# Kernel tuning notes

Measured on AMD Instinct MI355X. Metric: run time of the kernel, lower is better.

Reference implementation:

```python
import jax, jax.numpy as jnp
import numpy as np


def _gcn_conv(x, edge_index, W, b):
    """PyG GCNConv: add self-loops, symmetric normalization, scatter-add aggregation."""
    N = x.shape[0]
    loops = jnp.arange(N, dtype=edge_index.dtype)
    src = jnp.concatenate([edge_index[0], loops])  # [E+N]
    dst = jnp.concatenate([edge_index[1], loops])  # [E+N]
    # degree computed on destination nodes (flow: source_to_target)
    deg = jax.ops.segment_sum(jnp.ones_like(dst, dtype=x.dtype), dst, num_segments=N)
    deg_inv_sqrt = jnp.where(deg > 0, jax.lax.rsqrt(jnp.maximum(deg, 1.0)), 0.0)
    norm = deg_inv_sqrt[src] * deg_inv_sqrt[dst]  # [E+N]
    h = x @ W  # [N, out]
    msg = h[src] * norm[:, None]  # [E+N, out]
    out = jax.ops.segment_sum(msg, dst, num_segments=N)
    return out + b


def setup_inputs() -> dict:
    key = jax.random.key(0)
    k1, k2, k3, k4 = jax.random.split(key, 4)
    N, E, D_IN, D_HID, D_OUT = 100000, 1600000, 128, 128, 64
    x = jax.random.normal(k1, (N, D_IN), dtype=jnp.float32)
    edge_index = jax.random.randint(k2, (2, E), 0, N, dtype=jnp.int64)
    batch = jnp.zeros((N,), dtype=jnp.int64)
    W1 = jax.random.normal(k3, (D_IN, D_HID), dtype=jnp.float32) / np.sqrt(D_IN)
    b1 = jnp.zeros((D_HID,), dtype=jnp.float32)
    W2 = jax.random.normal(k4, (D_HID, D_OUT), dtype=jnp.float32) / np.sqrt(D_HID)
    b2 = jnp.zeros((D_OUT,), dtype=jnp.float32)
    return {"x": x, "edge_index": edge_index, "batch": batch,
            "W1": W1, "b1": b1, "W2": W2, "b2": b2}


def reference(x, edge_index, batch, W1, b1, W2, b2):
    h = _gcn_conv(x, edge_index, W1, b1)
    h = jax.nn.relu(h)
    # dropout is identity at inference (training=False)
    out = _gcn_conv(h, edge_index, W2, b2)
    # original computes F.log_softmax but discards it; returns out
    return out
```

## Files before the change

### kernel.cpp

```cpp
#include <hip/hip_runtime.h>
#include <hip/hip_fp16.h>


#define KDIM 128
#define BSHIFT 9
#define BSIZE 512
#define ECHUNK 2048
#define CAP 10240
#define PACK_SHIFT 20
#define PACK_MASK ((1u << PACK_SHIFT) - 1)

typedef _Float16 h8 __attribute__((ext_vector_type(8)));
typedef float f4v __attribute__((ext_vector_type(4)));


__launch_bounds__(256) __global__
void bscatter_kernel(const int* __restrict__ src, const int* __restrict__ dst,
                     int* __restrict__ ecnt, unsigned int* __restrict__ packed_out,
                     int E, int NB) {
    __shared__ int lcnt[256];
    __shared__ int lexc[256];
    __shared__ int lbase[256];
    __shared__ unsigned int lpacked[ECHUNK];
    __shared__ unsigned char lbslot[ECHUNK];

    const int t = threadIdx.x;
    lcnt[t] = 0;
    __syncthreads();

    const int base = blockIdx.x * ECHUNK;
    const int cnt = min(ECHUNK, E - base);

#pragma unroll
    for (int j = 0; j < ECHUNK / 256; j++) {
        int e = base + j * 256 + t;
        if (e < E) atomicAdd(&lcnt[dst[e] >> BSHIFT], 1);
    }
    __syncthreads();

    lexc[t] = lcnt[t];
    __syncthreads();
    for (int off = 1; off < 256; off <<= 1) {
        int x = (t >= off) ? lexc[t - off] : 0;
        __syncthreads();
        if (t >= off) lexc[t] += x;
        __syncthreads();
    }
    lexc[t] = lexc[t] - lcnt[t];

    if (t < NB && lcnt[t]) lbase[t] = t * CAP + atomicAdd(&ecnt[t], lcnt[t]);
    __syncthreads();
    lcnt[t] = lexc[t];
    __syncthreads();

#pragma unroll
    for (int j = 0; j < ECHUNK / 256; j++) {
        int e = base + j * 256 + t;
        if (e < E) {
            int d = dst[e];
            int b = d >> BSHIFT;
            int pos = atomicAdd(&lcnt[b], 1);
            lpacked[pos] = (unsigned int)src[e] | ((unsigned int)(d & (BSIZE - 1)) << PACK_SHIFT);
            lbslot[pos] = (unsigned char)b;
        }
    }
    __syncthreads();

#pragma unroll
    for (int j = 0; j < ECHUNK / 256; j++) {
        int s = j * 256 + t;
        if (s < cnt) {
            int b = lbslot[s];
            int pos = lbase[b] + (s - lexc[b]);
            if (pos < (b + 1) * CAP)
                packed_out[pos] = lpacked[s];
        }
    }
}


__launch_bounds__(1024) __global__
void bfinal_kernel(const unsigned int* __restrict__ packed, const int* __restrict__ ecnt,
                   int* __restrict__ rowptr, float* __restrict__ dinv,
                   int* __restrict__ ssrc, int N, int E, int NB) {
    __shared__ int ncnt[BSIZE];
    __shared__ int sbuf[BSIZE];
    __shared__ int bsc[256];
    __shared__ int bbase_sh;

    const int t = threadIdx.x;
    const int b = blockIdx.x;

    if (t < 256) bsc[t] = (t < NB) ? min(ecnt[t], CAP) : 0;
    if (t < BSIZE) ncnt[t] = 0;
    __syncthreads();

    const int cnt = min(ecnt[b], CAP);
    const unsigned int* pb = packed + (size_t)b * CAP;
    unsigned int held[CAP / 1024];
#pragma unroll
    for (int j = 0; j < CAP / 1024; j++) {
        int e = t + j * 1024;
        if (e < cnt) {
            unsigned int p = pb[e];
            held[j] = p;
            atomicAdd(&ncnt[p >> PACK_SHIFT], 1);
        }
    }

    __syncthreads();
    for (int off = 1; off < 256; off <<= 1) {
        int x = 0;
        if (t < 256 && t >= off) x = bsc[t - off];
        __syncthreads();
        if (t < 256 && t >= off) bsc[t] += x;
        __syncthreads();
    }
    if (t == 0) bbase_sh = (b == 0) ? 0 : bsc[b - 1];

    int mycnt = 0;
    if (t < BSIZE) {
        mycnt = ncnt[t];
        sbuf[t] = mycnt;
    }
    __syncthreads();
    for (int off = 1; off < BSIZE; off <<= 1) {
        int x = 0;
        if (t < BSIZE && t >= off) x = sbuf[t - off];
        __syncthreads();
        if (t < BSIZE && t >= off) sbuf[t] += x;
        __syncthreads();
    }

    const int gb = bbase_sh;
    if (t < BSIZE) {
        int exc = (t == 0) ? 0 : sbuf[t - 1];
        int node = (b << BSHIFT) + t;
        if (node < N) {
            rowptr[node] = gb + exc;
            dinv[node] = rsqrtf((float)(mycnt + 1));
        }
        ncnt[t] = gb + exc;
    }
    if (t == 0 && b == NB - 1) rowptr[N] = gb + cnt;
    __syncthreads();

#pragma unroll
    for (int j = 0; j < CAP / 1024; j++) {
        int e = t + j * 1024;
        if (e < cnt) {
            unsigned int p = held[j];
            int d = p >> PACK_SHIFT;
            int pos = atomicAdd(&ncnt[d], 1);
            ssrc[pos] = (int)(p & PACK_MASK);
        }
    }
}


__device__ inline h8 pack8(float4 u, float4 v) {
    h8 r;
    r[0] = (_Float16)u.x; r[1] = (_Float16)u.y; r[2] = (_Float16)u.z; r[3] = (_Float16)u.w;
    r[4] = (_Float16)v.x; r[5] = (_Float16)v.y; r[6] = (_Float16)v.z; r[7] = (_Float16)v.w;
    return r;
}

template <int DOUT, bool AHALF>
__launch_bounds__(256) __global__
void gemm_mfma_kernel(const void* __restrict__ Xv, const float* __restrict__ W,
                      const float* __restrict__ dinv, _Float16* __restrict__ outh, int N) {
    constexpr int K = KDIM;
    constexpr int KS = K + 8;
    constexpr int NT = DOUT / 16;
    __shared__ _Float16 Wl[DOUT * KS];

    const int t = threadIdx.x;
    const int wave = t >> 6;
    const int lane = t & 63;
    const int l15 = lane & 15;
    const int quad = lane >> 4;

#pragma unroll
    for (int i = t; i < DOUT * (K / 4); i += 256) {
        int n = i & (DOUT - 1);
        int kg = i / DOUT;
        union { _Float16 h[4]; uint2 u; } tmp;
#pragma unroll
        for (int j = 0; j < 4; j++)
            tmp.h[j] = (_Float16)W[(size_t)(kg * 4 + j) * DOUT + n];
        *(uint2*)(&Wl[n * KS + kg * 4]) = tmp.u;
    }
    __syncthreads();

    const int rowbase = blockIdx.x * 128;
    const int row0 = rowbase + wave * 32 + l15;
    const int row1 = row0 + 16;
    const int rc0 = min(row0, N - 1);
    const int rc1 = min(row1, N - 1);

    f4v acc[2][NT];
#pragma unroll
    for (int r = 0; r < 2; r++)
#pragma unroll
        for (int ct = 0; ct < NT; ct++) acc[r][ct] = (f4v)0.0f;

#pragma unroll
    for (int kc = 0; kc < K; kc += 32) {
        const int kof = kc + quad * 8;
        h8 a0, a1;
        if (AHALF) {
            const _Float16* Xh = (const _Float16*)Xv;
            a0 = *(const h8*)(Xh + (size_t)rc0 * K + kof);
            a1 = *(const h8*)(Xh + (size_t)rc1 * K + kof);
        } else {
            const float* Xf = (const float*)Xv;
            const float* p0 = Xf + (size_t)rc0 * K + kof;
            const float* p1 = Xf + (size_t)rc1 * K + kof;
            a0 = pack8(*(const float4*)p0, *(const float4*)(p0 + 4));
            a1 = pack8(*(const float4*)p1, *(const float4*)(p1 + 4));
        }
#pragma unroll
        for (int ct = 0; ct < NT; ct++) {
            h8 b = *(const h8*)(&Wl[(size_t)(ct * 16 + l15) * KS + kof]);
            acc[0][ct] = __builtin_amdgcn_mfma_f32_16x16x32_f16(a0, b, acc[0][ct], 0, 0, 0);
            acc[1][ct] = __builtin_amdgcn_mfma_f32_16x16x32_f16(a1, b, acc[1][ct], 0, 0, 0);
        }
    }

#pragma unroll
    for (int r = 0; r < 2; r++) {
        const int rb = rowbase + wave * 32 + r * 16 + quad * 4;
#pragma unroll
        for (int g = 0; g < 4; g++) {
            int row = rb + g;
            if (row < N) {
                float di = dinv[row];
                _Float16* op = outh + (size_t)row * DOUT + l15;
#pragma unroll
                for (int ct = 0; ct < NT; ct++)
                    op[ct * 16] = (_Float16)(acc[r][ct][g] * di);
            }
        }
    }
}


__launch_bounds__(512, 8) __global__
void agg_gemm_kernel(const __half* __restrict__ hs, const int* __restrict__ rowptr,
                     const int* __restrict__ ssrc, const float* __restrict__ dinv,
                     const float* __restrict__ bias, const float* __restrict__ W2,
                     _Float16* __restrict__ hs2, int N) {
    constexpr int K = KDIM;
    constexpr int KS = K + 8;
    constexpr int DO2 = 64;
    __shared__ _Float16 W2l[DO2 * KS];
    __shared__ _Float16 o_lds[8][4 * KS];

    const int t = threadIdx.x;

#pragma unroll
    for (int i = t; i < DO2 * (K / 4); i += 512) {
        int n = i & (DO2 - 1);
        int kg = i >> 6;
        union { _Float16 h[4]; uint2 u; } tmp;
#pragma unroll
        for (int j = 0; j < 4; j++)
            tmp.h[j] = (_Float16)W2[(size_t)(kg * 4 + j) * DO2 + n];
        *(uint2*)(&W2l[n * KS + kg * 4]) = tmp.u;
    }
    __syncthreads();

    const int nl = t >> 4;
    const int node = blockIdx.x * 32 + nl;
    const int flane = t & 15;
    const int c0 = flane * 8;

    h8 oh;
    if (node < N) {
        float acc[8];
        {
            uint4 u = *(const uint4*)(hs + (size_t)node * K + c0);
            const __half2* hp = (const __half2*)&u;
#pragma unroll
            for (int q = 0; q < 4; q++) {
                float2 f = __half22float2(hp[q]);
                acc[2 * q] = f.x;
                acc[2 * q + 1] = f.y;
            }
        }

        const int e0 = rowptr[node];
        const int e1 = rowptr[node + 1];
        int e = e0;
        for (; e + 4 <= e1; e += 4) {
            int s0 = ssrc[e + 0];
            int s1 = ssrc[e + 1];
            int s2 = ssrc[e + 2];
            int s3 = ssrc[e + 3];
            uint4 u0 = *(const uint4*)(hs + (size_t)s0 * K + c0);
            uint4 u1 = *(const uint4*)(hs + (size_t)s1 * K + c0);
            uint4 u2 = *(const uint4*)(hs + (size_t)s2 * K + c0);
            uint4 u3 = *(const uint4*)(hs + (size_t)s3 * K + c0);
            const __half2* p0 = (const __half2*)&u0;
            const __half2* p1 = (const __half2*)&u1;
            const __half2* p2 = (const __half2*)&u2;
            const __half2* p3 = (const __half2*)&u3;
#pragma unroll
            for (int q = 0; q < 4; q++) {
                float2 f0 = __half22float2(p0[q]);
                float2 f1 = __half22float2(p1[q]);
                float2 f2 = __half22float2(p2[q]);
                float2 f3 = __half22float2(p3[q]);
                acc[2 * q]     += (f0.x + f1.x) + (f2.x + f3.x);
                acc[2 * q + 1] += (f0.y + f1.y) + (f2.y + f3.y);
            }
        }
        for (; e < e1; e++) {
            int s = ssrc[e];
            uint4 u = *(const uint4*)(hs + (size_t)s * K + c0);
            const __half2* hp = (const __half2*)&u;
#pragma unroll
            for (int q = 0; q < 4; q++) {
                float2 f = __half22float2(hp[q]);
                acc[2 * q] += f.x;
                acc[2 * q + 1] += f.y;
            }
        }

        const float di = dinv[node];
#pragma unroll
        for (int q = 0; q < 2; q++) {
            float4 bq = *(const float4*)(bias + c0 + 4 * q);
            oh[4 * q + 0] = (_Float16)fmaxf(di * acc[4 * q + 0] + bq.x, 0.f);
            oh[4 * q + 1] = (_Float16)fmaxf(di * acc[4 * q + 1] + bq.y, 0.f);
            oh[4 * q + 2] = (_Float16)fmaxf(di * acc[4 * q + 2] + bq.z, 0.f);
            oh[4 * q + 3] = (_Float16)fmaxf(di * acc[4 * q + 3] + bq.w, 0.f);
        }
    } else {
#pragma unroll
        for (int j = 0; j < 8; j++) oh[j] = (_Float16)0.f;
    }

    const int wv = t >> 6;
    const int a = (t >> 4) & 3;
    *(h8*)(&o_lds[wv][a * KS + c0]) = oh;
    asm volatile("s_waitcnt lgkmcnt(0)" ::: "memory");
    __builtin_amdgcn_sched_barrier(0);

    const int lane = t & 63;
    const int l15 = lane & 15;
    const int quad = lane >> 4;

    f4v acc2[4];
#pragma unroll
    for (int ct = 0; ct < 4; ct++) acc2[ct] = (f4v)0.0f;

#pragma unroll
    for (int kc = 0; kc < K; kc += 32) {
        const int kof = kc + quad * 8;
        h8 afr = *(const h8*)(&o_lds[wv][(l15 & 3) * KS + kof]);
#pragma unroll
        for (int ct = 0; ct < 4; ct++) {
            h8 b = *(const h8*)(&W2l[(size_t)(ct * 16 + l15) * KS + kof]);
            acc2[ct] = __builtin_amdgcn_mfma_f32_16x16x32_f16(afr, b, acc2[ct], 0, 0, 0);
        }
    }

    f4v av = (quad == 0) ? acc2[0] : (quad == 1) ? acc2[1]
           : (quad == 2) ? acc2[2] : acc2[3];
    const int rowbase = blockIdx.x * 32 + wv * 4;
#pragma unroll
    for (int g = 0; g < 4; g++) {
        int r = rowbase + g;
        if (r < N)
            hs2[(size_t)r * DO2 + quad * 16 + l15] = (_Float16)(av[g] * dinv[r]);
    }
}


template <int DOUT, bool RELU, bool HOUT>
__launch_bounds__(256) __global__
void agg_kernel(const __half* __restrict__ hs, const int* __restrict__ rowptr,
                const int* __restrict__ ssrc, const float* __restrict__ dinv,
                const float* __restrict__ bias, void* __restrict__ outv, int N) {
    constexpr int TPN = DOUT / 8;
    const int npb = blockDim.x / TPN;
    const int node = blockIdx.x * npb + threadIdx.x / TPN;
    if (node >= N) return;
    const int lane = threadIdx.x % TPN;
    const int c0 = lane * 8;

    float acc[8];
    {
        uint4 u = *(const uint4*)(hs + (size_t)node * DOUT + c0);
        const __half2* hp = (const __half2*)&u;
#pragma unroll
        for (int q = 0; q < 4; q++) {
            float2 f = __half22float2(hp[q]);
            acc[2 * q] = f.x;
            acc[2 * q + 1] = f.y;
        }
    }

    const int e0 = rowptr[node];
    const int e1 = rowptr[node + 1];
    int e = e0;
    for (; e + 4 <= e1; e += 4) {
        int s0 = ssrc[e + 0];
        int s1 = ssrc[e + 1];
        int s2 = ssrc[e + 2];
        int s3 = ssrc[e + 3];
        uint4 u0 = *(const uint4*)(hs + (size_t)s0 * DOUT + c0);
        uint4 u1 = *(const uint4*)(hs + (size_t)s1 * DOUT + c0);
        uint4 u2 = *(const uint4*)(hs + (size_t)s2 * DOUT + c0);
        uint4 u3 = *(const uint4*)(hs + (size_t)s3 * DOUT + c0);
        const __half2* p0 = (const __half2*)&u0;
        const __half2* p1 = (const __half2*)&u1;
        const __half2* p2 = (const __half2*)&u2;
        const __half2* p3 = (const __half2*)&u3;
#pragma unroll
        for (int q = 0; q < 4; q++) {
            float2 f0 = __half22float2(p0[q]);
            float2 f1 = __half22float2(p1[q]);
            float2 f2 = __half22float2(p2[q]);
            float2 f3 = __half22float2(p3[q]);
            acc[2 * q]     += (f0.x + f1.x) + (f2.x + f3.x);
            acc[2 * q + 1] += (f0.y + f1.y) + (f2.y + f3.y);
        }
    }
    for (; e < e1; e++) {
        int s = ssrc[e];
        uint4 u = *(const uint4*)(hs + (size_t)s * DOUT + c0);
        const __half2* hp = (const __half2*)&u;
#pragma unroll
        for (int q = 0; q < 4; q++) {
            float2 f = __half22float2(hp[q]);
            acc[2 * q] += f.x;
            acc[2 * q + 1] += f.y;
        }
    }

    const float di = dinv[node];
    float o[8];
#pragma unroll
    for (int q = 0; q < 2; q++) {
        float4 bq = *(const float4*)(bias + c0 + 4 * q);
        o[4 * q + 0] = di * acc[4 * q + 0] + bq.x;
        o[4 * q + 1] = di * acc[4 * q + 1] + bq.y;
        o[4 * q + 2] = di * acc[4 * q + 2] + bq.z;
        o[4 * q + 3] = di * acc[4 * q + 3] + bq.w;
    }
    if (RELU) {
#pragma unroll
        for (int j = 0; j < 8; j++) o[j] = fmaxf(o[j], 0.f);
    }
    if (HOUT) {
        union { __half2 h[4]; uint4 u; } pk;
#pragma unroll
        for (int q = 0; q < 4; q++)
            pk.h[q] = __floats2half2_rn(o[2 * q], o[2 * q + 1]);
        *(uint4*)((__half*)outv + (size_t)node * DOUT + c0) = pk.u;
    } else {
        float* op = (float*)outv + (size_t)node * DOUT + c0;
        *(float4*)op = make_float4(o[0], o[1], o[2], o[3]);
        *(float4*)(op + 4) = make_float4(o[4], o[5], o[6], o[7]);
    }
}


extern "C" void kernel_launch(void* const* d_in, const int* in_sizes, int n_in,
                              void* d_out, int out_size, void* d_ws, size_t ws_size,
                              hipStream_t stream) {
    const float* x  = (const float*)d_in[0];
    const int*   ei = (const int*)d_in[1];
    const float* W1 = (const float*)d_in[3];
    const float* b1 = (const float*)d_in[4];
    const float* W2 = (const float*)d_in[5];
    const float* b2 = (const float*)d_in[6];
    float* out = (float*)d_out;

    const int N = in_sizes[0] / KDIM;
    const int E = in_sizes[1] / 2;
    const int* esrc = ei;
    const int* edst = ei + E;
    const int NB = (N + BSIZE - 1) >> BSHIFT;

    char* ws = (char*)d_ws;
    size_t off = 0;
    auto alloc = [&](size_t bytes) {
        size_t p = off;
        off = (off + bytes + 511) & ~(size_t)511;
        return p;
    };
    int*      ecnt    = (int*)(ws + alloc((size_t)NB * 4));
    int*      rowptr  = (int*)(ws + alloc((size_t)(N + 1) * 4));
    float*    dinv    = (float*)(ws + alloc((size_t)N * 4));
    int*      ssrc    = (int*)(ws + alloc((size_t)E * 4));
    _Float16* hs1     = (_Float16*)(ws + alloc((size_t)N * KDIM * 2));
    _Float16* hs2     = (_Float16*)(ws + alloc((size_t)N * 64 * 2));
    unsigned int* packed = (unsigned int*)hs1;
    (void)ws_size; (void)n_in; (void)out_size;

    const int eb = (E + ECHUNK - 1) / ECHUNK;

    hipMemsetAsync(ecnt, 0, (size_t)NB * 4, stream);

    bscatter_kernel<<<eb, 256, 0, stream>>>(esrc, edst, ecnt, packed, E, NB);
    bfinal_kernel<<<NB, 1024, 0, stream>>>(packed, ecnt, rowptr, dinv, ssrc, N, E, NB);

    gemm_mfma_kernel<128, false><<<(N + 127) / 128, 256, 0, stream>>>(x, W1, dinv, hs1, N);

    agg_gemm_kernel<<<(N + 31) / 32, 512, 0, stream>>>(
        (const __half*)hs1, rowptr, ssrc, dinv, b1, W2, hs2, N);

    agg_kernel<64, false, false><<<(N + 31) / 32, 256, 0, stream>>>(
        (const __half*)hs2, rowptr, ssrc, dinv, b2, out, N);
}
```

Before: 254.8 us.

## Merge layer-1 GEMM with edge bucket scatter into one interleaved launch

Combines the first dense GEMM and the edge bucketing scatter into a single prep kernel whose blocks alternate between the two roles, so the compute-heavy and atomic-heavy work can run concurrently. To remove the GEMM's dependency on the degree array, the source-side normalization moves into the first aggregation kernel, which now gathers dinv per source edge. The packed edge buffer is relocated to the second hidden buffer so it does not alias the GEMM output. This adds per-edge dinv loads in aggregation and a shared 34 KB LDS footprint for both roles, which may limit occupancy.

```diff
diff --git a/kernel.cpp b/kernel.cpp
--- a/kernel.cpp
+++ b/kernel.cpp
@@ -13,67 +13,156 @@
 typedef _Float16 h8 __attribute__((ext_vector_type(8)));
 typedef float f4v __attribute__((ext_vector_type(4)));
 
+__device__ inline h8 pack8(float4 u, float4 v) {
+    h8 r;
+    r[0] = (_Float16)u.x; r[1] = (_Float16)u.y; r[2] = (_Float16)u.z; r[3] = (_Float16)u.w;
+    r[4] = (_Float16)v.x; r[5] = (_Float16)v.y; r[6] = (_Float16)v.z; r[7] = (_Float16)v.w;
+    return r;
+}
+
 
 __launch_bounds__(256) __global__
-void bscatter_kernel(const int* __restrict__ src, const int* __restrict__ dst,
-                     int* __restrict__ ecnt, unsigned int* __restrict__ packed_out,
-                     int E, int NB) {
-    __shared__ int lcnt[256];
-    __shared__ int lexc[256];
-    __shared__ int lbase[256];
-    __shared__ unsigned int lpacked[ECHUNK];
-    __shared__ unsigned char lbslot[ECHUNK];
+void prep_kernel(const float* __restrict__ X, const float* __restrict__ W,
+                 _Float16* __restrict__ outh,
+                 const int* __restrict__ src, const int* __restrict__ dst,
+                 int* __restrict__ ecnt, unsigned int* __restrict__ packed_out,
+                 int N, int E, int NB, int GB, int EB) {
+    __shared__ __align__(16) char shbuf[34816];
 
     const int t = threadIdx.x;
-    lcnt[t] = 0;
-    __syncthreads();
-
-    const int base = blockIdx.x * ECHUNK;
-    const int cnt = min(ECHUNK, E - base);
-
-#pragma unroll
-    for (int j = 0; j < ECHUNK / 256; j++) {
-        int e = base + j * 256 + t;
-        if (e < E) atomicAdd(&lcnt[dst[e] >> BSHIFT], 1);
-    }
-    __syncthreads();
-
-    lexc[t] = lcnt[t];
-    __syncthreads();
-    for (int off = 1; off < 256; off <<= 1) {
-        int x = (t >= off) ? lexc[t - off] : 0;
-        __syncthreads();
-        if (t >= off) lexc[t] += x;
-        __syncthreads();
-    }
-    lexc[t] = lexc[t] - lcnt[t];
-
-    if (t < NB && lcnt[t]) lbase[t] = t * CAP + atomicAdd(&ecnt[t], lcnt[t]);
-    __syncthreads();
-    lcnt[t] = lexc[t];
-    __syncthreads();
-
-#pragma unroll
-    for (int j = 0; j < ECHUNK / 256; j++) {
-        int e = base + j * 256 + t;
-        if (e < E) {
-            int d = dst[e];
-            int b = d >> BSHIFT;
-            int pos = atomicAdd(&lcnt[b], 1);
-            lpacked[pos] = (unsigned int)src[e] | ((unsigned int)(d & (BSIZE - 1)) << PACK_SHIFT);
-            lbslot[pos] = (unsigned char)b;
-        }
-    }
-    __syncthreads();
-
-#pragma unroll
-    for (int j = 0; j < ECHUNK / 256; j++) {
-        int s = j * 256 + t;
-        if (s < cnt) {
-            int b = lbslot[s];
-            int pos = lbase[b] + (s - lexc[b]);
-            if (pos < (b + 1) * CAP)
-                packed_out[pos] = lpacked[s];
+    const int tm = 2 * min(GB, EB);
+    bool isg;
+    int bid;
+    if ((int)blockIdx.x < tm) {
+        isg = !(blockIdx.x & 1);
+        bid = blockIdx.x >> 1;
+    } else {
+        bid = (tm >> 1) + ((int)blockIdx.x - tm);
+        isg = (GB > EB);
+    }
+
+    if (isg) {
+        constexpr int K = KDIM;
+        constexpr int KS = K + 8;
+        constexpr int DOUT = 128;
+        constexpr int NT = DOUT / 16;
+        _Float16* Wl = (_Float16*)shbuf;
+
+        const int wave = t >> 6;
+        const int lane = t & 63;
+        const int l15 = lane & 15;
+        const int quad = lane >> 4;
+
+#pragma unroll
+        for (int i = t; i < DOUT * (K / 4); i += 256) {
+            int n = i & (DOUT - 1);
+            int kg = i >> 7;
+            union { _Float16 h[4]; uint2 u; } tmp;
+#pragma unroll
+            for (int j = 0; j < 4; j++)
+                tmp.h[j] = (_Float16)W[(size_t)(kg * 4 + j) * DOUT + n];
+            *(uint2*)(&Wl[n * KS + kg * 4]) = tmp.u;
+        }
+        __syncthreads();
+
+        const int rowbase = bid * 128;
+        const int row0 = rowbase + wave * 32 + l15;
+        const int row1 = row0 + 16;
+        const int rc0 = min(row0, N - 1);
+        const int rc1 = min(row1, N - 1);
+
+        f4v acc[2][NT];
+#pragma unroll
+        for (int r = 0; r < 2; r++)
+#pragma unroll
+            for (int ct = 0; ct < NT; ct++) acc[r][ct] = (f4v)0.0f;
+
+#pragma unroll
+        for (int kc = 0; kc < K; kc += 32) {
+            const int kof = kc + quad * 8;
+            const float* p0 = X + (size_t)rc0 * K + kof;
+            const float* p1 = X + (size_t)rc1 * K + kof;
+            h8 a0 = pack8(*(const float4*)p0, *(const float4*)(p0 + 4));
+            h8 a1 = pack8(*(const float4*)p1, *(const float4*)(p1 + 4));
+#pragma unroll
+            for (int ct = 0; ct < NT; ct++) {
+                h8 b = *(const h8*)(&Wl[(size_t)(ct * 16 + l15) * KS + kof]);
+                acc[0][ct] = __builtin_amdgcn_mfma_f32_16x16x32_f16(a0, b, acc[0][ct], 0, 0, 0);
+                acc[1][ct] = __builtin_amdgcn_mfma_f32_16x16x32_f16(a1, b, acc[1][ct], 0, 0, 0);
+            }
+        }
+
+#pragma unroll
+        for (int r = 0; r < 2; r++) {
+            const int rb = rowbase + wave * 32 + r * 16 + quad * 4;
+#pragma unroll
+            for (int g = 0; g < 4; g++) {
+                int row = rb + g;
+                if (row < N) {
+                    _Float16* op = outh + (size_t)row * DOUT + l15;
+#pragma unroll
+                    for (int ct = 0; ct < NT; ct++)
+                        op[ct * 16] = (_Float16)acc[r][ct][g];
+                }
+            }
+        }
+    } else {
+        int* lcnt = (int*)shbuf;
+        int* lexc = lcnt + 256;
+        int* lbase = lexc + 256;
+        unsigned int* lpacked = (unsigned int*)(lbase + 256);
+        unsigned char* lbslot = (unsigned char*)(lpacked + ECHUNK);
+
+        lcnt[t] = 0;
+        __syncthreads();
+
+        const int base = bid * ECHUNK;
+        const int cnt = min(ECHUNK, E - base);
+
+#pragma unroll
+        for (int j = 0; j < ECHUNK / 256; j++) {
+            int e = base + j * 256 + t;
+            if (e < E) atomicAdd(&lcnt[dst[e] >> BSHIFT], 1);
+        }
+        __syncthreads();
+
+        lexc[t] = lcnt[t];
+        __syncthreads();
+        for (int off = 1; off < 256; off <<= 1) {
+            int x = (t >= off) ? lexc[t - off] : 0;
+            __syncthreads();
+            if (t >= off) lexc[t] += x;
+            __syncthreads();
+        }
+        lexc[t] = lexc[t] - lcnt[t];
+
+        if (t < NB && lcnt[t]) lbase[t] = t * CAP + atomicAdd(&ecnt[t], lcnt[t]);
+        __syncthreads();
+        lcnt[t] = lexc[t];
+        __syncthreads();
+
+#pragma unroll
+        for (int j = 0; j < ECHUNK / 256; j++) {
+            int e = base + j * 256 + t;
+            if (e < E) {
+                int d = dst[e];
+                int b = d >> BSHIFT;
+                int pos = atomicAdd(&lcnt[b], 1);
+                lpacked[pos] = (unsigned int)src[e] | ((unsigned int)(d & (BSIZE - 1)) << PACK_SHIFT);
+                lbslot[pos] = (unsigned char)b;
+            }
+        }
+        __syncthreads();
+
+#pragma unroll
+        for (int j = 0; j < ECHUNK / 256; j++) {
+            int s = j * 256 + t;
+            if (s < cnt) {
+                int b = lbslot[s];
+                int pos = lbase[b] + (s - lexc[b]);
+                if (pos < (b + 1) * CAP)
+                    packed_out[pos] = lpacked[s];
+            }
         }
     }
 }
@@ -153,93 +242,6 @@
             int d = p >> PACK_SHIFT;
             int pos = atomicAdd(&ncnt[d], 1);
             ssrc[pos] = (int)(p & PACK_MASK);
-        }
-    }
-}
-
-
-__device__ inline h8 pack8(float4 u, float4 v) {
-    h8 r;
-    r[0] = (_Float16)u.x; r[1] = (_Float16)u.y; r[2] = (_Float16)u.z; r[3] = (_Float16)u.w;
-    r[4] = (_Float16)v.x; r[5] = (_Float16)v.y; r[6] = (_Float16)v.z; r[7] = (_Float16)v.w;
-    return r;
-}
-
-template <int DOUT, bool AHALF>
-__launch_bounds__(256) __global__
-void gemm_mfma_kernel(const void* __restrict__ Xv, const float* __restrict__ W,
-                      const float* __restrict__ dinv, _Float16* __restrict__ outh, int N) {
-    constexpr int K = KDIM;
-    constexpr int KS = K + 8;
-    constexpr int NT = DOUT / 16;
-    __shared__ _Float16 Wl[DOUT * KS];
-
-    const int t = threadIdx.x;
-    const int wave = t >> 6;
-    const int lane = t & 63;
-    const int l15 = lane & 15;
-    const int quad = lane >> 4;
-
-#pragma unroll
-    for (int i = t; i < DOUT * (K / 4); i += 256) {
-        int n = i & (DOUT - 1);
-        int kg = i / DOUT;
-        union { _Float16 h[4]; uint2 u; } tmp;
-#pragma unroll
-        for (int j = 0; j < 4; j++)
-            tmp.h[j] = (_Float16)W[(size_t)(kg * 4 + j) * DOUT + n];
-        *(uint2*)(&Wl[n * KS + kg * 4]) = tmp.u;
-    }
-    __syncthreads();
-
-    const int rowbase = blockIdx.x * 128;
-    const int row0 = rowbase + wave * 32 + l15;
-    const int row1 = row0 + 16;
-    const int rc0 = min(row0, N - 1);
-    const int rc1 = min(row1, N - 1);
-
-    f4v acc[2][NT];
-#pragma unroll
-    for (int r = 0; r < 2; r++)
-#pragma unroll
-        for (int ct = 0; ct < NT; ct++) acc[r][ct] = (f4v)0.0f;
-
-#pragma unroll
-    for (int kc = 0; kc < K; kc += 32) {
-        const int kof = kc + quad * 8;
-        h8 a0, a1;
-        if (AHALF) {
-            const _Float16* Xh = (const _Float16*)Xv;
-            a0 = *(const h8*)(Xh + (size_t)rc0 * K + kof);
-            a1 = *(const h8*)(Xh + (size_t)rc1 * K + kof);
-        } else {
-            const float* Xf = (const float*)Xv;
-            const float* p0 = Xf + (size_t)rc0 * K + kof;
-            const float* p1 = Xf + (size_t)rc1 * K + kof;
-            a0 = pack8(*(const float4*)p0, *(const float4*)(p0 + 4));
-            a1 = pack8(*(const float4*)p1, *(const float4*)(p1 + 4));
-        }
-#pragma unroll
-        for (int ct = 0; ct < NT; ct++) {
-            h8 b = *(const h8*)(&Wl[(size_t)(ct * 16 + l15) * KS + kof]);
-            acc[0][ct] = __builtin_amdgcn_mfma_f32_16x16x32_f16(a0, b, acc[0][ct], 0, 0, 0);
-            acc[1][ct] = __builtin_amdgcn_mfma_f32_16x16x32_f16(a1, b, acc[1][ct], 0, 0, 0);
-        }
-    }
-
-#pragma unroll
-    for (int r = 0; r < 2; r++) {
-        const int rb = rowbase + wave * 32 + r * 16 + quad * 4;
-#pragma unroll
-        for (int g = 0; g < 4; g++) {
-            int row = rb + g;
-            if (row < N) {
-                float di = dinv[row];
-                _Float16* op = outh + (size_t)row * DOUT + l15;
-#pragma unroll
-                for (int ct = 0; ct < NT; ct++)
-                    op[ct * 16] = (_Float16)(acc[r][ct][g] * di);
-            }
         }
     }
 }
@@ -277,6 +279,7 @@
 
     h8 oh;
     if (node < N) {
+        const float di = dinv[node];
         float acc[8];
         {
             uint4 u = *(const uint4*)(hs + (size_t)node * K + c0);
@@ -284,8 +287,8 @@
 #pragma unroll
             for (int q = 0; q < 4; q++) {
                 float2 f = __half22float2(hp[q]);
-                acc[2 * q] = f.x;
-                acc[2 * q + 1] = f.y;
+                acc[2 * q]     = di * f.x;
+                acc[2 * q + 1] = di * f.y;
             }
         }
 
@@ -297,6 +300,10 @@
             int s1 = ssrc[e + 1];
             int s2 = ssrc[e + 2];
             int s3 = ssrc[e + 3];
+            float d0 = dinv[s0];
+            float d1 = dinv[s1];
+            float d2 = dinv[s2];
+            float d3 = dinv[s3];
             uint4 u0 = *(const uint4*)(hs + (size_t)s0 * K + c0);
             uint4 u1 = *(const uint4*)(hs + (size_t)s1 * K + c0);
             uint4 u2 = *(const uint4*)(hs + (size_t)s2 * K + c0);
@@ -311,23 +318,23 @@
                 float2 f1 = __half22float2(p1[q]);
                 float2 f2 = __half22float2(p2[q]);
                 float2 f3 = __half22float2(p3[q]);
-                acc[2 * q]     += (f0.x + f1.x) + (f2.x + f3.x);
-                acc[2 * q + 1] += (f0.y + f1.y) + (f2.y + f3.y);
+                acc[2 * q]     += d0 * f0.x + d1 * f1.x + d2 * f2.x + d3 * f3.x;
+                acc[2 * q + 1] += d0 * f0.y + d1 * f1.y + d2 * f2.y + d3 * f3.y;
             }
         }
         for (; e < e1; e++) {
             int s = ssrc[e];
+            float ds = dinv[s];
             uint4 u = *(const uint4*)(hs + (size_t)s * K + c0);
             const __half2* hp = (const __half2*)&u;
 #pragma unroll
             for (int q = 0; q < 4; q++) {
                 float2 f = __half22float2(hp[q]);
-                acc[2 * q] += f.x;
-                acc[2 * q + 1] += f.y;
-            }
-        }
-
-        const float di = dinv[node];
+                acc[2 * q]     += ds * f.x;
+                acc[2 * q + 1] += ds * f.y;
+            }
+        }
+
 #pragma unroll
         for (int q = 0; q < 2; q++) {
             float4 bq = *(const float4*)(bias + c0 + 4 * q);
@@ -498,17 +505,17 @@
     int*      ssrc    = (int*)(ws + alloc((size_t)E * 4));
     _Float16* hs1     = (_Float16*)(ws + alloc((size_t)N * KDIM * 2));
     _Float16* hs2     = (_Float16*)(ws + alloc((size_t)N * 64 * 2));
-    unsigned int* packed = (unsigned int*)hs1;
+    unsigned int* packed = (unsigned int*)hs2;
     (void)ws_size; (void)n_in; (void)out_size;
 
     const int eb = (E + ECHUNK - 1) / ECHUNK;
+    const int gb = (N + 127) / 128;
 
     hipMemsetAsync(ecnt, 0, (size_t)NB * 4, stream);
 
-    bscatter_kernel<<<eb, 256, 0, stream>>>(esrc, edst, ecnt, packed, E, NB);
+    prep_kernel<<<gb + eb, 256, 0, stream>>>(x, W1, hs1, esrc, edst, ecnt,
+                                             packed, N, E, NB, gb, eb);
     bfinal_kernel<<<NB, 1024, 0, stream>>>(packed, ecnt, rowptr, dinv, ssrc, N, E, NB);
-
-    gemm_mfma_kernel<128, false><<<(N + 127) / 128, 256, 0, stream>>>(x, W1, dinv, hs1, N);
 
     agg_gemm_kernel<<<(N + 31) / 32, 512, 0, stream>>>(
         (const __half*)hs1, rowptr, ssrc, dinv, b1, W2, hs2, N);
```

After: 246.1 us (median of 2 runs). 1.04x faster.
